# Performance work log

Measured on AMD Instinct MI355X. Metric: run time of the kernel, lower is better.

The kernel has to match this reference:

```python
import jax, jax.numpy as jnp
import numpy as np

K = 4096          # in_features
N = 11008         # out_features
GROUP = 128       # scale group size along K
PACK = 16
BATCH, SEQ = 2, 4096


def setup_inputs() -> dict:
    key = jax.random.key(0)
    k1, k2, k3, k4 = jax.random.split(key, 4)
    x = jax.random.normal(k1, (BATCH, SEQ, K), dtype=jnp.float16)
    # valid ternary codes in {0,1,2} encoding w = code - 1 in {-1,0,+1}
    codes = jax.random.randint(k2, (K, N), 0, 3, dtype=jnp.int32)
    codes = codes.reshape(K // PACK, PACK, N)
    shifts = (2 * jnp.arange(PACK, dtype=jnp.int32))[None, :, None]
    packed_weight = jnp.sum(codes << shifts, axis=1).astype(jnp.int32)  # (K//16, N)
    scales = (jax.random.uniform(k3, (K // GROUP, N), dtype=jnp.float32) * 0.1 + 0.01).astype(jnp.float16)
    bias = (jax.random.normal(k4, (N,), dtype=jnp.float32) * 0.01).astype(jnp.float16)
    return {"x": x, "packed_weight": packed_weight, "scales": scales, "bias": bias}


def _dequant(packed_weight, scales):
    # unpack 16 two-bit codes per int32 along K
    shifts = (2 * jnp.arange(PACK, dtype=jnp.int32))[None, :, None]
    codes = (packed_weight[:, None, :] >> shifts) & 3        # (K//16, 16, N)
    Kp = packed_weight.shape[0] * PACK
    Nn = packed_weight.shape[1]
    w = (codes.astype(jnp.float16) - jnp.float16(1.0)).reshape(Kp, Nn)  # ternary {-1,0,1}
    scale_full = jnp.repeat(scales, GROUP, axis=0)            # (K, N) group-wise gamma
    return w * scale_full


def reference(x, packed_weight, scales, bias):
    Kp = packed_weight.shape[0] * PACK
    Nn = packed_weight.shape[1]
    w = _dequant(packed_weight, scales)                       # (K, N) fp16
    x2 = x.reshape(-1, Kp).astype(jnp.float16)                # (M, K)
    out = jnp.dot(x2, w, preferred_element_type=jnp.float32).astype(jnp.float16)
    out = out + bias
    return out.reshape(*x.shape[:-1], Nn)
```

## Files before the change

### kernel.cpp

```cpp
#include <hip/hip_runtime.h>
#include <stdint.h>

#define K_DIM 4096
#define N_DIM 11008
#define M_DIM 8192
#define BM 256
#define BN 128
#define BK 64
#define NSLAB (K_DIM / BK)
#define BSTRIDE 72

#define FBM 128
#define FBK 32
#define FASTRIDE 32
#define FBSTRIDE 40

typedef _Float16 half8  __attribute__((ext_vector_type(8)));
typedef _Float16 half2v __attribute__((ext_vector_type(2)));
typedef float    floatx4 __attribute__((ext_vector_type(4)));

#define WS_NEEDED ((size_t)M_DIM * K_DIM * 2)

__device__ __forceinline__ void async_lds16(const void* g, void* l) {
    __builtin_amdgcn_global_load_lds(
        (const __attribute__((address_space(1))) uint32_t*)g,
        (__attribute__((address_space(3))) uint32_t*)l, 16, 0, 0);
}

__global__ __launch_bounds__(256) void cvt_a(const float* __restrict__ x,
                                             _Float16* __restrict__ xh) {
    const size_t i = ((size_t)blockIdx.x * 256 + threadIdx.x) * 8;
    const float4 a = *(const float4*)(x + i);
    const float4 b = *(const float4*)(x + i + 4);
    half8 h;
    h[0] = (_Float16)a.x; h[1] = (_Float16)a.y; h[2] = (_Float16)a.z; h[3] = (_Float16)a.w;
    h[4] = (_Float16)b.x; h[5] = (_Float16)b.y; h[6] = (_Float16)b.z; h[7] = (_Float16)b.w;
    *(half8*)(xh + i) = h;
}

__global__ __launch_bounds__(512, 4) void ternary_gemm_hy(
    const _Float16* __restrict__ xh,
    const int*   __restrict__ pw,
    const float* __restrict__ scales,
    const float* __restrict__ bias,
    float*       __restrict__ out)
{
    __shared__ __align__(16) _Float16 lds_a[BM * BK];
    __shared__ __align__(16) _Float16 lds_b[BN * BSTRIDE];

    const int tid  = threadIdx.x;
    const int lane = tid & 63;
    const int wave = tid >> 6;

    const int n0 = blockIdx.x * BN;
    const int m0 = blockIdx.y * BM;
    const int wm = (wave & 3) * 64;
    const int wn = (wave >> 2) * 64;

    const _Float16* ga[4];
    _Float16* la[4];
    #pragma unroll
    for (int i = 0; i < 4; ++i) {
        const int idx = tid + i * 512;
        const int row = idx >> 3;
        const int c   = idx & 7;
        ga[i] = xh + (size_t)(m0 + row) * K_DIM + ((c ^ (row & 7)) * 8);
        la[i] = lds_a + idx * 8;
    }

    const int nb = tid >> 2;
    const int kp = tid & 3;
    const int*   pwp = pw + (size_t)kp * N_DIM + n0 + nb;
    const float* scp = scales + n0 + nb;
    _Float16* bl = lds_b + nb * BSTRIDE + kp * 16;

    floatx4 acc[4][4];
    #pragma unroll
    for (int i = 0; i < 4; ++i)
        #pragma unroll
        for (int j = 0; j < 4; ++j)
            acc[i][j] = floatx4{0.f, 0.f, 0.f, 0.f};

    const int lr = lane & 15;
    const int g  = lane >> 4;
    const int qk = g * 8;
    const int r7 = lr & 7;

    int abase[4], bbase[4];
    #pragma unroll
    for (int t = 0; t < 4; ++t) {
        abase[t] = (wm + t * 16 + lr) * BK;
        bbase[t] = (wn + t * 16 + lr) * BSTRIDE + qk;
    }

    for (int slab = 0; slab < NSLAB; ++slab) {
        const int k0 = slab * BK;

        #pragma unroll
        for (int i = 0; i < 4; ++i)
            async_lds16(ga[i] + k0, la[i]);

        uint32_t v  = (uint32_t)pwp[(size_t)slab * 4 * N_DIM];
        _Float16 sh = (_Float16)scp[(size_t)(slab >> 1) * N_DIM];
        uint32_t sbits = (uint32_t)__builtin_bit_cast(unsigned short, sh);
        uint32_t tmpl = sbits | (((sbits >> 8) ^ 0x80u) << 24);

        uint32_t q[8];
        #pragma unroll
        for (int j = 0; j < 8; ++j) {
            uint32_t t4 = (v >> (4 * j)) & 0xFu;
            uint32_t sp = (t4 | (t4 << 14)) & 0x00030003u;
            uint32_t sel = ((sp & 0x00010001u) << 1) | ((0x00030003u - sp) << 8);
            q[j] = __builtin_amdgcn_perm(tmpl, tmpl, sel);
        }
        *(uint4*)(bl)     = make_uint4(q[0], q[1], q[2], q[3]);
        *(uint4*)(bl + 8) = make_uint4(q[4], q[5], q[6], q[7]);

        __syncthreads();

        #pragma unroll
        for (int h = 0; h < 2; ++h) {
            half8 af[4], bfr[4];
            #pragma unroll
            for (int t = 0; t < 4; ++t) {
                af[t]  = *(const half8*)&lds_a[abase[t] + (((h * 4 + g) ^ r7) * 8)];
                bfr[t] = *(const half8*)&lds_b[bbase[t] + h * 32];
            }
            #pragma unroll
            for (int mt = 0; mt < 4; ++mt)
                #pragma unroll
                for (int nt = 0; nt < 4; ++nt)
                    acc[mt][nt] = __builtin_amdgcn_mfma_f32_16x16x32_f16(
                        af[mt], bfr[nt], acc[mt][nt], 0, 0, 0);
        }

        __syncthreads();
    }

    float bv[4];
    #pragma unroll
    for (int nt = 0; nt < 4; ++nt) bv[nt] = bias[n0 + wn + nt * 16 + lr];

    const int rbase = g * 4;
    #pragma unroll
    for (int mt = 0; mt < 4; ++mt) {
        #pragma unroll
        for (int nt = 0; nt < 4; ++nt) {
            const int col = n0 + wn + nt * 16 + lr;
            float* op = out + (size_t)(m0 + wm + mt * 16 + rbase) * N_DIM + col;
            floatx4 a = acc[mt][nt];
            #pragma unroll
            for (int r = 0; r < 4; ++r)
                op[(size_t)r * N_DIM] = a[r] + bv[nt];
        }
    }
}

__global__ __launch_bounds__(256, 2) void ternary_gemm(
    const float* __restrict__ x,
    const int*   __restrict__ pw,
    const float* __restrict__ scales,
    const float* __restrict__ bias,
    float*       __restrict__ out)
{
    __shared__ __align__(16) _Float16 lds_a[FBM * FASTRIDE];
    __shared__ __align__(16) _Float16 lds_b[FBM * FBSTRIDE];

    const int tid  = threadIdx.x;
    const int lane = tid & 63;
    const int wave = tid >> 6;

    const int n0 = blockIdx.x * FBM;
    const int m0 = blockIdx.y * FBM;

    const int wm = (wave & 1) * 64;
    const int wn = (wave >> 1) * 64;

    const int nb  = tid & 127;
    const int kpi = tid >> 7;
    const int*   pwp = pw + (size_t)kpi * N_DIM + n0 + nb;
    const float* scp = scales + n0 + nb;
    _Float16* bl = lds_b + nb * FBSTRIDE + kpi * 16;

    floatx4 acc[4][4];
    #pragma unroll
    for (int i = 0; i < 4; ++i)
        #pragma unroll
        for (int j = 0; j < 4; ++j)
            acc[i][j] = floatx4{0.f, 0.f, 0.f, 0.f};

    const int lr = lane & 15;
    const int qk = (lane >> 4) * 8;

    for (int slab = 0; slab < K_DIM / FBK; ++slab) {
        const int k0 = slab * FBK;

        #pragma unroll
        for (int i = 0; i < 4; ++i) {
            const int idx = tid + i * 256;
            const int row = idx >> 3;
            const int kq  = (idx & 7) * 4;
            float4 v4 = *(const float4*)(x + (size_t)(m0 + row) * K_DIM + k0 + kq);
            half2v h0; h0[0] = (_Float16)v4.x; h0[1] = (_Float16)v4.y;
            half2v h1; h1[0] = (_Float16)v4.z; h1[1] = (_Float16)v4.w;
            *(uint2*)(lds_a + row * FASTRIDE + kq) =
                make_uint2(__builtin_bit_cast(uint32_t, h0),
                           __builtin_bit_cast(uint32_t, h1));
        }

        uint32_t v  = (uint32_t)pwp[(size_t)slab * 2 * N_DIM];
        _Float16 sh = (_Float16)scp[(size_t)(slab >> 2) * N_DIM];
        uint32_t sbits = (uint32_t)__builtin_bit_cast(unsigned short, sh);
        uint32_t tmpl = sbits | (((sbits >> 8) ^ 0x80u) << 24);

        uint32_t q[8];
        #pragma unroll
        for (int j = 0; j < 8; ++j) {
            uint32_t t4 = (v >> (4 * j)) & 0xFu;
            uint32_t sp = (t4 | (t4 << 14)) & 0x00030003u;
            uint32_t sel = ((sp & 0x00010001u) << 1) | ((0x00030003u - sp) << 8);
            q[j] = __builtin_amdgcn_perm(tmpl, tmpl, sel);
        }
        *(uint4*)(bl)     = make_uint4(q[0], q[1], q[2], q[3]);
        *(uint4*)(bl + 8) = make_uint4(q[4], q[5], q[6], q[7]);

        __syncthreads();

        half8 af[4], bfr[4];
        #pragma unroll
        for (int t = 0; t < 4; ++t) {
            af[t]  = *(const half8*)&lds_a[(wm + t * 16 + lr) * FASTRIDE + qk];
            bfr[t] = *(const half8*)&lds_b[(wn + t * 16 + lr) * FBSTRIDE + qk];
        }
        #pragma unroll
        for (int mt = 0; mt < 4; ++mt)
            #pragma unroll
            for (int nt = 0; nt < 4; ++nt)
                acc[mt][nt] = __builtin_amdgcn_mfma_f32_16x16x32_f16(
                    af[mt], bfr[nt], acc[mt][nt], 0, 0, 0);

        __syncthreads();
    }

    float bv[4];
    #pragma unroll
    for (int nt = 0; nt < 4; ++nt) bv[nt] = bias[n0 + wn + nt * 16 + lr];

    const int rbase = (lane >> 4) * 4;
    #pragma unroll
    for (int mt = 0; mt < 4; ++mt) {
        #pragma unroll
        for (int nt = 0; nt < 4; ++nt) {
            const int col = n0 + wn + nt * 16 + lr;
            float* op = out + (size_t)(m0 + wm + mt * 16 + rbase) * N_DIM + col;
            floatx4 a = acc[mt][nt];
            #pragma unroll
            for (int r = 0; r < 4; ++r)
                op[(size_t)r * N_DIM] = a[r] + bv[nt];
        }
    }
}

extern "C" void kernel_launch(void* const* d_in, const int* in_sizes, int n_in,
                              void* d_out, int out_size, void* d_ws, size_t ws_size,
                              hipStream_t stream) {
    const float* x  = (const float*)d_in[0];
    const int*   pw = (const int*)d_in[1];
    const float* sc = (const float*)d_in[2];
    const float* bs = (const float*)d_in[3];
    float* out = (float*)d_out;

    if (d_ws != nullptr && ws_size >= WS_NEEDED) {
        _Float16* xh = (_Float16*)d_ws;
        cvt_a<<<dim3((unsigned)((size_t)M_DIM * K_DIM / (256 * 8))), 256, 0, stream>>>(x, xh);
        ternary_gemm_hy<<<dim3(N_DIM / BN, M_DIM / BM), 512, 0, stream>>>(xh, pw, sc, bs, out);
    } else {
        ternary_gemm<<<dim3(N_DIM / FBM, M_DIM / FBM), 256, 0, stream>>>(x, pw, sc, bs, out);
    }
}
```

Before: 1.128 ms.

## Double-buffer LDS with 256x256 tiles, weight prefetch and grid swizzle

Replaces the single-buffered 256x128 GEMM with a 256x256-tile kernel. It double-buffers both the A and B LDS tiles and prefetches packed ternary weights and scales two slabs ahead in registers. Each iteration's global-to-LDS loads and weight unpacking now overlap with MFMA work on the other buffer, using fine-grained vmcnt waits instead of two full barriers per slab. It also adds an XOR-swizzled B layout in place of a padded stride, a 1D grid swizzle for L2 locality, and raised MFMA priority. In exchange it uses about 128KB of LDS and more accumulator registers per block, which lowers occupancy to roughly one workgroup per CU.

After: 1.269 ms. +12.5%, slower.

```diff
diff --git a/kernel.cpp b/kernel.cpp
--- a/kernel.cpp
+++ b/kernel.cpp
@@ -5,10 +5,12 @@
 #define N_DIM 11008
 #define M_DIM 8192
 #define BM 256
-#define BN 128
+#define BN 256
 #define BK 64
 #define NSLAB (K_DIM / BK)
-#define BSTRIDE 72
+#define ABUF (BM * BK)
+#define BBUF (BN * BK)
+#define NWG ((N_DIM / BN) * (M_DIM / BM))
 
 #define FBM 128
 #define FBK 32
@@ -38,74 +40,60 @@
     *(half8*)(xh + i) = h;
 }
 
-__global__ __launch_bounds__(512, 4) void ternary_gemm_hy(
+__global__ __launch_bounds__(512, 2) void ternary_gemm_db(
     const _Float16* __restrict__ xh,
     const int*   __restrict__ pw,
     const float* __restrict__ scales,
     const float* __restrict__ bias,
     float*       __restrict__ out)
 {
-    __shared__ __align__(16) _Float16 lds_a[BM * BK];
-    __shared__ __align__(16) _Float16 lds_b[BN * BSTRIDE];
+    __shared__ __align__(16) _Float16 lds_a[2 * ABUF];
+    __shared__ __align__(16) _Float16 lds_b[2 * BBUF];
 
     const int tid  = threadIdx.x;
     const int lane = tid & 63;
-    const int wave = tid >> 6;
-
-    const int n0 = blockIdx.x * BN;
-    const int m0 = blockIdx.y * BM;
-    const int wm = (wave & 3) * 64;
-    const int wn = (wave >> 2) * 64;
-
-    const _Float16* ga[4];
-    _Float16* la[4];
-    #pragma unroll
-    for (int i = 0; i < 4; ++i) {
-        const int idx = tid + i * 512;
-        const int row = idx >> 3;
-        const int c   = idx & 7;
-        ga[i] = xh + (size_t)(m0 + row) * K_DIM + ((c ^ (row & 7)) * 8);
-        la[i] = lds_a + idx * 8;
-    }
-
-    const int nb = tid >> 2;
-    const int kp = tid & 3;
-    const int*   pwp = pw + (size_t)kp * N_DIM + n0 + nb;
+    const int w    = tid >> 6;
+
+    const int bid = blockIdx.x;
+    const int swz = (bid & 7) * (NWG / 8) + (bid >> 3);
+    const int n0 = (swz % (N_DIM / BN)) * BN;
+    const int m0 = (swz / (N_DIM / BN)) * BM;
+
+    const int band = (w & 3) * 64;
+    const int wn   = (w >> 2) * 128;
+
+    const int arow = lane >> 3;
+    const int achk = (lane & 7) ^ arow;
+    const _Float16* gaBase = xh + (size_t)(m0 + band + arow) * K_DIM + achk * 8;
+
+    const int nb = tid >> 1;
+    const int kp = tid & 1;
+    const int* pwp = pw + (size_t)(kp * 2) * N_DIM + n0 + nb;
     const float* scp = scales + n0 + nb;
-    _Float16* bl = lds_b + nb * BSTRIDE + kp * 16;
-
-    floatx4 acc[4][4];
+    const int s7  = nb & 7;
+    const int c0a = ((kp * 2 + 0) * 2 + 0) ^ s7;
+    const int c0b = ((kp * 2 + 0) * 2 + 1) ^ s7;
+    const int c1a = ((kp * 2 + 1) * 2 + 0) ^ s7;
+    const int c1b = ((kp * 2 + 1) * 2 + 1) ^ s7;
+
+    floatx4 acc[4][8];
     #pragma unroll
     for (int i = 0; i < 4; ++i)
         #pragma unroll
-        for (int j = 0; j < 4; ++j)
+        for (int j = 0; j < 8; ++j)
             acc[i][j] = floatx4{0.f, 0.f, 0.f, 0.f};
 
     const int lr = lane & 15;
     const int g  = lane >> 4;
-    const int qk = g * 8;
-    const int r7 = lr & 7;
-
-    int abase[4], bbase[4];
-    #pragma unroll
-    for (int t = 0; t < 4; ++t) {
-        abase[t] = (wm + t * 16 + lr) * BK;
-        bbase[t] = (wn + t * 16 + lr) * BSTRIDE + qk;
-    }
-
-    for (int slab = 0; slab < NSLAB; ++slab) {
-        const int k0 = slab * BK;
-
-        #pragma unroll
-        for (int i = 0; i < 4; ++i)
-            async_lds16(ga[i] + k0, la[i]);
-
-        uint32_t v  = (uint32_t)pwp[(size_t)slab * 4 * N_DIM];
-        _Float16 sh = (_Float16)scp[(size_t)(slab >> 1) * N_DIM];
-        uint32_t sbits = (uint32_t)__builtin_bit_cast(unsigned short, sh);
-        uint32_t tmpl = sbits | (((sbits >> 8) ^ 0x80u) << 24);
-
-        uint32_t q[8];
+    const int x7 = lr & 7;
+
+    int aoff[4], boff[8];
+    #pragma unroll
+    for (int mt = 0; mt < 4; ++mt) aoff[mt] = (band + mt * 16 + lr) * BK;
+    #pragma unroll
+    for (int nt = 0; nt < 8; ++nt) boff[nt] = (wn + nt * 16 + lr) * BK;
+
+    auto permq = [](uint32_t v, uint32_t tmpl, uint32_t* q) {
         #pragma unroll
         for (int j = 0; j < 8; ++j) {
             uint32_t t4 = (v >> (4 * j)) & 0xFu;
@@ -113,41 +101,95 @@
             uint32_t sel = ((sp & 0x00010001u) << 1) | ((0x00030003u - sp) << 8);
             q[j] = __builtin_amdgcn_perm(tmpl, tmpl, sel);
         }
-        *(uint4*)(bl)     = make_uint4(q[0], q[1], q[2], q[3]);
-        *(uint4*)(bl + 8) = make_uint4(q[4], q[5], q[6], q[7]);
-
-        __syncthreads();
-
+    };
+    auto stage_b = [&](uint32_t v0, uint32_t v1, float scf, _Float16* rowb) {
+        _Float16 sh = (_Float16)scf;
+        uint32_t sbits = (uint32_t)__builtin_bit_cast(unsigned short, sh);
+        uint32_t tmpl = sbits | (((sbits >> 8) ^ 0x80u) << 24);
+        uint32_t q[8];
+        permq(v0, tmpl, q);
+        *(uint4*)(rowb + c0a * 8) = make_uint4(q[0], q[1], q[2], q[3]);
+        *(uint4*)(rowb + c0b * 8) = make_uint4(q[4], q[5], q[6], q[7]);
+        permq(v1, tmpl, q);
+        *(uint4*)(rowb + c1a * 8) = make_uint4(q[0], q[1], q[2], q[3]);
+        *(uint4*)(rowb + c1b * 8) = make_uint4(q[4], q[5], q[6], q[7]);
+    };
+    auto stage_a = [&](int slab, int buf) {
+        const _Float16* gk = gaBase + slab * BK;
+        _Float16* dst = lds_a + buf * ABUF + band * BK;
+        #pragma unroll
+        for (int i = 0; i < 8; ++i)
+            async_lds16(gk + (size_t)i * 8 * K_DIM, dst + i * 8 * BK);
+    };
+
+    uint32_t pv00 = (uint32_t)pwp[0];
+    uint32_t pv01 = (uint32_t)pwp[(size_t)1 * N_DIM];
+    float    sc0  = scp[0];
+    uint32_t pvA0 = (uint32_t)pwp[(size_t)4 * N_DIM];
+    uint32_t pvA1 = (uint32_t)pwp[(size_t)5 * N_DIM];
+    float    scA  = scp[0];
+    stage_a(0, 0);
+    stage_b(pv00, pv01, sc0, lds_b + nb * BK);
+    asm volatile("s_waitcnt lgkmcnt(0)" ::: "memory");
+    __builtin_amdgcn_s_barrier();
+
+    uint32_t pvB0 = 0, pvB1 = 0; float scB = 0.f;
+
+    for (int t = 0; t < NSLAB; ++t) {
+        const int cur = t & 1;
+
+        if (t + 2 < NSLAB) {
+            pvB0 = (uint32_t)pwp[(size_t)((t + 2) * 4 + 0) * N_DIM];
+            pvB1 = (uint32_t)pwp[(size_t)((t + 2) * 4 + 1) * N_DIM];
+            scB  = scp[(size_t)((t + 2) >> 1) * N_DIM];
+        }
+        if (t + 1 < NSLAB) {
+            stage_a(t + 1, cur ^ 1);
+            stage_b(pvA0, pvA1, scA, lds_b + (cur ^ 1) * BBUF + nb * BK);
+        }
+
+        if (t + 2 < NSLAB)      asm volatile("s_waitcnt vmcnt(11)" ::: "memory");
+        else if (t + 1 < NSLAB) asm volatile("s_waitcnt vmcnt(8)"  ::: "memory");
+        else                    asm volatile("s_waitcnt vmcnt(0)"  ::: "memory");
+
+        const _Float16* Ab = lds_a + cur * ABUF;
+        const _Float16* Bb = lds_b + cur * BBUF;
+        __builtin_amdgcn_s_setprio(1);
         #pragma unroll
         for (int h = 0; h < 2; ++h) {
-            half8 af[4], bfr[4];
-            #pragma unroll
-            for (int t = 0; t < 4; ++t) {
-                af[t]  = *(const half8*)&lds_a[abase[t] + (((h * 4 + g) ^ r7) * 8)];
-                bfr[t] = *(const half8*)&lds_b[bbase[t] + h * 32];
-            }
+            const int co = ((h * 4 + g) ^ x7) * 8;
+            half8 af[4], bf[8];
+            #pragma unroll
+            for (int mt = 0; mt < 4; ++mt) af[mt] = *(const half8*)&Ab[aoff[mt] + co];
+            #pragma unroll
+            for (int nt = 0; nt < 8; ++nt) bf[nt] = *(const half8*)&Bb[boff[nt] + co];
             #pragma unroll
             for (int mt = 0; mt < 4; ++mt)
                 #pragma unroll
-                for (int nt = 0; nt < 4; ++nt)
+                for (int nt = 0; nt < 8; ++nt)
                     acc[mt][nt] = __builtin_amdgcn_mfma_f32_16x16x32_f16(
-                        af[mt], bfr[nt], acc[mt][nt], 0, 0, 0);
-        }
-
-        __syncthreads();
-    }
-
-    float bv[4];
-    #pragma unroll
-    for (int nt = 0; nt < 4; ++nt) bv[nt] = bias[n0 + wn + nt * 16 + lr];
+                        af[mt], bf[nt], acc[mt][nt], 0, 0, 0);
+        }
+        __builtin_amdgcn_s_setprio(0);
+
+        if (t + 1 < NSLAB) {
+            asm volatile("s_waitcnt lgkmcnt(0)" ::: "memory");
+            __builtin_amdgcn_s_barrier();
+        }
+        pvA0 = pvB0; pvA1 = pvB1; scA = scB;
+    }
+
+    float bv[8];
+    #pragma unroll
+    for (int nt = 0; nt < 8; ++nt) bv[nt] = bias[n0 + wn + nt * 16 + lr];
 
     const int rbase = g * 4;
     #pragma unroll
     for (int mt = 0; mt < 4; ++mt) {
         #pragma unroll
-        for (int nt = 0; nt < 4; ++nt) {
+        for (int nt = 0; nt < 8; ++nt) {
             const int col = n0 + wn + nt * 16 + lr;
-            float* op = out + (size_t)(m0 + wm + mt * 16 + rbase) * N_DIM + col;
+            float* op = out + (size_t)(m0 + band + mt * 16 + rbase) * N_DIM + col;
             floatx4 a = acc[mt][nt];
             #pragma unroll
             for (int r = 0; r < 4; ++r)
@@ -273,7 +315,7 @@
     if (d_ws != nullptr && ws_size >= WS_NEEDED) {
         _Float16* xh = (_Float16*)d_ws;
         cvt_a<<<dim3((unsigned)((size_t)M_DIM * K_DIM / (256 * 8))), 256, 0, stream>>>(x, xh);
-        ternary_gemm_hy<<<dim3(N_DIM / BN, M_DIM / BM), 512, 0, stream>>>(xh, pw, sc, bs, out);
+        ternary_gemm_db<<<dim3(NWG), 512, 0, stream>>>(xh, pw, sc, bs, out);
     } else {
         ternary_gemm<<<dim3(N_DIM / FBM, M_DIM / FBM), 256, 0, stream>>>(x, pw, sc, bs, out);
     }
```

## Switch to 32x32x16 MFMA, XOR-swizzled B tile, block-id remap, prefetch weights

Applied to the files above, without the earlier changes.

Replaces the 4x4 grid of 16x16x32 MFMAs per wave with a 2x2 grid of 32x32x16 MFMAs. This reduces LDS fragment loads per MFMA and the instruction count. The padded B tile in LDS becomes an XOR-swizzled layout that matches the A swizzle, which avoids bank conflicts without padding. The grid becomes 1D with a block-id remap that groups blocks for L2 reuse. The packed weight and scale for the next slab are now loaded one iteration ahead to hide global latency. The epilogue is rewritten for the 32x32 accumulator layout, which changes the output store pattern.

Result: slower. 1.183 ms (+4.8%).

```diff
diff --git a/kernel.cpp b/kernel.cpp
--- a/kernel.cpp
+++ b/kernel.cpp
@@ -8,16 +8,19 @@
 #define BN 128
 #define BK 64
 #define NSLAB (K_DIM / BK)
-#define BSTRIDE 72
+#define NBN (N_DIM / BN)
+#define NBM (M_DIM / BM)
+#define NWG (NBN * NBM)
 
 #define FBM 128
 #define FBK 32
 #define FASTRIDE 32
 #define FBSTRIDE 40
 
-typedef _Float16 half8  __attribute__((ext_vector_type(8)));
-typedef _Float16 half2v __attribute__((ext_vector_type(2)));
+typedef _Float16 half8   __attribute__((ext_vector_type(8)));
+typedef _Float16 half2v  __attribute__((ext_vector_type(2)));
 typedef float    floatx4 __attribute__((ext_vector_type(4)));
+typedef float    floatx16 __attribute__((ext_vector_type(16)));
 
 #define WS_NEEDED ((size_t)M_DIM * K_DIM * 2)
 
@@ -38,7 +41,7 @@
     *(half8*)(xh + i) = h;
 }
 
-__global__ __launch_bounds__(512, 4) void ternary_gemm_hy(
+__global__ __launch_bounds__(512, 4) void ternary_gemm_w3(
     const _Float16* __restrict__ xh,
     const int*   __restrict__ pw,
     const float* __restrict__ scales,
@@ -46,16 +49,19 @@
     float*       __restrict__ out)
 {
     __shared__ __align__(16) _Float16 lds_a[BM * BK];
-    __shared__ __align__(16) _Float16 lds_b[BN * BSTRIDE];
+    __shared__ __align__(16) _Float16 lds_b[BN * BK];
 
     const int tid  = threadIdx.x;
     const int lane = tid & 63;
-    const int wave = tid >> 6;
-
-    const int n0 = blockIdx.x * BN;
-    const int m0 = blockIdx.y * BM;
-    const int wm = (wave & 3) * 64;
-    const int wn = (wave >> 2) * 64;
+    const int w    = tid >> 6;
+
+    const int bid = blockIdx.x;
+    const int swz = (bid & 7) * (NWG / 8) + (bid >> 3);
+    const int m0 = (swz / NBN) * BM;
+    const int n0 = (swz % NBN) * BN;
+
+    const int wm = (w & 3) * 64;
+    const int wn = (w >> 2) * 64;
 
     const _Float16* ga[4];
     _Float16* la[4];
@@ -70,88 +76,93 @@
 
     const int nb = tid >> 2;
     const int kp = tid & 3;
-    const int*   pwp = pw + (size_t)kp * N_DIM + n0 + nb;
+    const int* pwp = pw + (size_t)kp * N_DIM + n0 + nb;
     const float* scp = scales + n0 + nb;
-    _Float16* bl = lds_b + nb * BSTRIDE + kp * 16;
-
-    floatx4 acc[4][4];
-    #pragma unroll
-    for (int i = 0; i < 4; ++i)
-        #pragma unroll
-        for (int j = 0; j < 4; ++j)
-            acc[i][j] = floatx4{0.f, 0.f, 0.f, 0.f};
-
-    const int lr = lane & 15;
-    const int g  = lane >> 4;
-    const int qk = g * 8;
-    const int r7 = lr & 7;
-
-    int abase[4], bbase[4];
-    #pragma unroll
-    for (int t = 0; t < 4; ++t) {
-        abase[t] = (wm + t * 16 + lr) * BK;
-        bbase[t] = (wn + t * 16 + lr) * BSTRIDE + qk;
-    }
-
-    for (int slab = 0; slab < NSLAB; ++slab) {
-        const int k0 = slab * BK;
-
+    const int s7 = nb & 7;
+    const int cA = (kp * 2 + 0) ^ s7;
+    const int cB = (kp * 2 + 1) ^ s7;
+    _Float16* bl = lds_b + nb * BK;
+
+    floatx16 acc[2][2];
+    #pragma unroll
+    for (int i = 0; i < 2; ++i)
+        #pragma unroll
+        for (int j = 0; j < 2; ++j)
+            acc[i][j] = (floatx16)(0.f);
+
+    const int l31 = lane & 31;
+    const int h5  = lane >> 5;
+    const int r7  = l31 & 7;
+
+    const int aoff0 = (wm +  0 + l31) * BK;
+    const int aoff1 = (wm + 32 + l31) * BK;
+    const int boff0 = (wn +  0 + l31) * BK;
+    const int boff1 = (wn + 32 + l31) * BK;
+
+    uint32_t pv = (uint32_t)pwp[0];
+    float    sv = scp[0];
+
+    for (int t = 0; t < NSLAB; ++t) {
         #pragma unroll
         for (int i = 0; i < 4; ++i)
-            async_lds16(ga[i] + k0, la[i]);
-
-        uint32_t v  = (uint32_t)pwp[(size_t)slab * 4 * N_DIM];
-        _Float16 sh = (_Float16)scp[(size_t)(slab >> 1) * N_DIM];
-        uint32_t sbits = (uint32_t)__builtin_bit_cast(unsigned short, sh);
-        uint32_t tmpl = sbits | (((sbits >> 8) ^ 0x80u) << 24);
-
-        uint32_t q[8];
-        #pragma unroll
-        for (int j = 0; j < 8; ++j) {
-            uint32_t t4 = (v >> (4 * j)) & 0xFu;
-            uint32_t sp = (t4 | (t4 << 14)) & 0x00030003u;
-            uint32_t sel = ((sp & 0x00010001u) << 1) | ((0x00030003u - sp) << 8);
-            q[j] = __builtin_amdgcn_perm(tmpl, tmpl, sel);
-        }
-        *(uint4*)(bl)     = make_uint4(q[0], q[1], q[2], q[3]);
-        *(uint4*)(bl + 8) = make_uint4(q[4], q[5], q[6], q[7]);
-
-        __syncthreads();
-
-        #pragma unroll
-        for (int h = 0; h < 2; ++h) {
-            half8 af[4], bfr[4];
-            #pragma unroll
-            for (int t = 0; t < 4; ++t) {
-                af[t]  = *(const half8*)&lds_a[abase[t] + (((h * 4 + g) ^ r7) * 8)];
-                bfr[t] = *(const half8*)&lds_b[bbase[t] + h * 32];
+            async_lds16(ga[i] + t * BK, la[i]);
+
+        uint32_t pvN = pv; float svN = sv;
+        if (t + 1 < NSLAB) {
+            pvN = (uint32_t)pwp[(size_t)(t + 1) * 4 * N_DIM];
+            svN = scp[(size_t)((t + 1) >> 1) * N_DIM];
+        }
+
+        {
+            _Float16 sh = (_Float16)sv;
+            uint32_t sbits = (uint32_t)__builtin_bit_cast(unsigned short, sh);
+            uint32_t tmpl = sbits | (((sbits >> 8) ^ 0x80u) << 24);
+            uint32_t q[8];
+            #pragma unroll
+            for (int j = 0; j < 8; ++j) {
+                uint32_t t4 = (pv >> (4 * j)) & 0xFu;
+                uint32_t sp = (t4 | (t4 << 14)) & 0x00030003u;
+                uint32_t sel = ((sp & 0x00010001u) << 1) | ((0x00030003u - sp) << 8);
+                q[j] = __builtin_amdgcn_perm(tmpl, tmpl, sel);
             }
-            #pragma unroll
-            for (int mt = 0; mt < 4; ++mt)
-                #pragma unroll
-                for (int nt = 0; nt < 4; ++nt)
-                    acc[mt][nt] = __builtin_amdgcn_mfma_f32_16x16x32_f16(
-                        af[mt], bfr[nt], acc[mt][nt], 0, 0, 0);
-        }
-
-        __syncthreads();
-    }
-
-    float bv[4];
-    #pragma unroll
-    for (int nt = 0; nt < 4; ++nt) bv[nt] = bias[n0 + wn + nt * 16 + lr];
-
-    const int rbase = g * 4;
-    #pragma unroll
-    for (int mt = 0; mt < 4; ++mt) {
-        #pragma unroll
-        for (int nt = 0; nt < 4; ++nt) {
-            const int col = n0 + wn + nt * 16 + lr;
-            float* op = out + (size_t)(m0 + wm + mt * 16 + rbase) * N_DIM + col;
-            floatx4 a = acc[mt][nt];
-            #pragma unroll
-            for (int r = 0; r < 4; ++r)
-                op[(size_t)r * N_DIM] = a[r] + bv[nt];
+            *(uint4*)(bl + cA * 8) = make_uint4(q[0], q[1], q[2], q[3]);
+            *(uint4*)(bl + cB * 8) = make_uint4(q[4], q[5], q[6], q[7]);
+        }
+
+        __syncthreads();
+
+        #pragma unroll
+        for (int ks = 0; ks < 4; ++ks) {
+            const int ck = ((ks * 2 + h5) ^ r7) * 8;
+            half8 af0 = *(const half8*)&lds_a[aoff0 + ck];
+            half8 af1 = *(const half8*)&lds_a[aoff1 + ck];
+            half8 bf0 = *(const half8*)&lds_b[boff0 + ck];
+            half8 bf1 = *(const half8*)&lds_b[boff1 + ck];
+            acc[0][0] = __builtin_amdgcn_mfma_f32_32x32x16_f16(af0, bf0, acc[0][0], 0, 0, 0);
+            acc[0][1] = __builtin_amdgcn_mfma_f32_32x32x16_f16(af0, bf1, acc[0][1], 0, 0, 0);
+            acc[1][0] = __builtin_amdgcn_mfma_f32_32x32x16_f16(af1, bf0, acc[1][0], 0, 0, 0);
+            acc[1][1] = __builtin_amdgcn_mfma_f32_32x32x16_f16(af1, bf1, acc[1][1], 0, 0, 0);
+        }
+
+        __syncthreads();
+        pv = pvN; sv = svN;
+    }
+
+    float bvE[2];
+    #pragma unroll
+    for (int nt = 0; nt < 2; ++nt) bvE[nt] = bias[n0 + wn + nt * 32 + l31];
+
+    #pragma unroll
+    for (int mt = 0; mt < 2; ++mt) {
+        #pragma unroll
+        for (int nt = 0; nt < 2; ++nt) {
+            const int col = n0 + wn + nt * 32 + l31;
+            const floatx16 a = acc[mt][nt];
+            #pragma unroll
+            for (int reg = 0; reg < 16; ++reg) {
+                const int row = m0 + wm + mt * 32 + (reg & 3) + 8 * (reg >> 2) + 4 * h5;
+                out[(size_t)row * N_DIM + col] = a[reg] + bvE[nt];
+            }
         }
     }
 }
@@ -273,7 +284,7 @@
     if (d_ws != nullptr && ws_size >= WS_NEEDED) {
         _Float16* xh = (_Float16*)d_ws;
         cvt_a<<<dim3((unsigned)((size_t)M_DIM * K_DIM / (256 * 8))), 256, 0, stream>>>(x, xh);
-        ternary_gemm_hy<<<dim3(N_DIM / BN, M_DIM / BM), 512, 0, stream>>>(xh, pw, sc, bs, out);
+        ternary_gemm_w3<<<dim3(NWG), 512, 0, stream>>>(xh, pw, sc, bs, out);
     } else {
         ternary_gemm<<<dim3(N_DIM / FBM, M_DIM / FBM), 256, 0, stream>>>(x, pw, sc, bs, out);
     }
```

## Double-buffer A tile in LDS, prefetch packed weights, and swizzle workgroup order

Applied to the files above, without the earlier changes.

The main GEMM now double-buffers the activation tile in LDS, issuing the async global-to-LDS loads for the next K slab before computing the current one. It also prefetches the packed weights and scales two slabs ahead in registers. The loop uses explicit vmcnt/lgkmcnt waits and raw s_barrier in place of __syncthreads. The B tile drops its padded stride for an XOR-swizzled layout, the launch becomes a 1D grid remapped for L2 locality, and s_setprio raises priority during the MFMA section. The costs are extra LDS for the second A buffer and hand-tuned wait counts that must match the number of outstanding loads exactly.

Measured after the change: 1.070 ms, median of 2. -5.2%, faster.

```diff
diff --git a/kernel.cpp b/kernel.cpp
--- a/kernel.cpp
+++ b/kernel.cpp
@@ -8,15 +8,18 @@
 #define BN 128
 #define BK 64
 #define NSLAB (K_DIM / BK)
-#define BSTRIDE 72
+#define NBN (N_DIM / BN)
+#define NBM (M_DIM / BM)
+#define NWG (NBN * NBM)
+#define ABUF (BM * BK)
 
 #define FBM 128
 #define FBK 32
 #define FASTRIDE 32
 #define FBSTRIDE 40
 
-typedef _Float16 half8  __attribute__((ext_vector_type(8)));
-typedef _Float16 half2v __attribute__((ext_vector_type(2)));
+typedef _Float16 half8   __attribute__((ext_vector_type(8)));
+typedef _Float16 half2v  __attribute__((ext_vector_type(2)));
 typedef float    floatx4 __attribute__((ext_vector_type(4)));
 
 #define WS_NEEDED ((size_t)M_DIM * K_DIM * 2)
@@ -38,41 +41,47 @@
     *(half8*)(xh + i) = h;
 }
 
-__global__ __launch_bounds__(512, 4) void ternary_gemm_hy(
+__global__ __launch_bounds__(512, 4) void ternary_gemm_p2(
     const _Float16* __restrict__ xh,
     const int*   __restrict__ pw,
     const float* __restrict__ scales,
     const float* __restrict__ bias,
     float*       __restrict__ out)
 {
-    __shared__ __align__(16) _Float16 lds_a[BM * BK];
-    __shared__ __align__(16) _Float16 lds_b[BN * BSTRIDE];
+    __shared__ __align__(16) _Float16 lds_a[2 * ABUF];
+    __shared__ __align__(16) _Float16 lds_b[BN * BK];
 
     const int tid  = threadIdx.x;
     const int lane = tid & 63;
-    const int wave = tid >> 6;
-
-    const int n0 = blockIdx.x * BN;
-    const int m0 = blockIdx.y * BM;
-    const int wm = (wave & 3) * 64;
-    const int wn = (wave >> 2) * 64;
+    const int w    = tid >> 6;
+
+    const int bid = blockIdx.x;
+    const int swz = (bid & 7) * (NWG / 8) + (bid >> 3);
+    const int m0 = (swz / NBN) * BM;
+    const int n0 = (swz % NBN) * BN;
+
+    const int band = (w & 3) * 64;
+    const int wn   = (w >> 2) * 64;
 
     const _Float16* ga[4];
-    _Float16* la[4];
+    int laOff[4];
     #pragma unroll
     for (int i = 0; i < 4; ++i) {
         const int idx = tid + i * 512;
         const int row = idx >> 3;
         const int c   = idx & 7;
-        ga[i] = xh + (size_t)(m0 + row) * K_DIM + ((c ^ (row & 7)) * 8);
-        la[i] = lds_a + idx * 8;
+        ga[i]    = xh + (size_t)(m0 + row) * K_DIM + ((c ^ (row & 7)) * 8);
+        laOff[i] = idx * 8;
     }
 
     const int nb = tid >> 2;
     const int kp = tid & 3;
-    const int*   pwp = pw + (size_t)kp * N_DIM + n0 + nb;
+    const int* pwp = pw + (size_t)kp * N_DIM + n0 + nb;
     const float* scp = scales + n0 + nb;
-    _Float16* bl = lds_b + nb * BSTRIDE + kp * 16;
+    const int s7 = nb & 7;
+    const int cA = (kp * 2 + 0) ^ s7;
+    const int cB = (kp * 2 + 1) ^ s7;
+    _Float16* bl = lds_b + nb * BK;
 
     floatx4 acc[4][4];
     #pragma unroll
@@ -83,28 +92,24 @@
 
     const int lr = lane & 15;
     const int g  = lane >> 4;
-    const int qk = g * 8;
-    const int r7 = lr & 7;
-
-    int abase[4], bbase[4];
+    const int x7 = lr & 7;
+
+    int aoff[4], boff[4];
     #pragma unroll
     for (int t = 0; t < 4; ++t) {
-        abase[t] = (wm + t * 16 + lr) * BK;
-        bbase[t] = (wn + t * 16 + lr) * BSTRIDE + qk;
-    }
-
-    for (int slab = 0; slab < NSLAB; ++slab) {
-        const int k0 = slab * BK;
-
+        aoff[t] = (band + t * 16 + lr) * BK;
+        boff[t] = (wn   + t * 16 + lr) * BK;
+    }
+
+    auto stage_a = [&](int t, int buf) {
         #pragma unroll
         for (int i = 0; i < 4; ++i)
-            async_lds16(ga[i] + k0, la[i]);
-
-        uint32_t v  = (uint32_t)pwp[(size_t)slab * 4 * N_DIM];
-        _Float16 sh = (_Float16)scp[(size_t)(slab >> 1) * N_DIM];
+            async_lds16(ga[i] + t * BK, lds_a + buf * ABUF + laOff[i]);
+    };
+    auto stage_b = [&](uint32_t v, float scf) {
+        _Float16 sh = (_Float16)scf;
         uint32_t sbits = (uint32_t)__builtin_bit_cast(unsigned short, sh);
         uint32_t tmpl = sbits | (((sbits >> 8) ^ 0x80u) << 24);
-
         uint32_t q[8];
         #pragma unroll
         for (int j = 0; j < 8; ++j) {
@@ -113,18 +118,44 @@
             uint32_t sel = ((sp & 0x00010001u) << 1) | ((0x00030003u - sp) << 8);
             q[j] = __builtin_amdgcn_perm(tmpl, tmpl, sel);
         }
-        *(uint4*)(bl)     = make_uint4(q[0], q[1], q[2], q[3]);
-        *(uint4*)(bl + 8) = make_uint4(q[4], q[5], q[6], q[7]);
-
-        __syncthreads();
-
+        *(uint4*)(bl + cA * 8) = make_uint4(q[0], q[1], q[2], q[3]);
+        *(uint4*)(bl + cB * 8) = make_uint4(q[4], q[5], q[6], q[7]);
+    };
+
+    stage_a(0, 0);
+    uint32_t pv0 = (uint32_t)pwp[0];
+    float    sv0 = scp[0];
+    uint32_t pv1 = (uint32_t)pwp[(size_t)4 * N_DIM];
+    float    sv1 = scp[0];
+
+    for (int t = 0; t < NSLAB; ++t) {
+        const int cur = t & 1;
+
+        if (t + 1 < NSLAB) stage_a(t + 1, cur ^ 1);
+        uint32_t pv2 = 0; float sv2 = 0.f;
+        if (t + 2 < NSLAB) {
+            pv2 = (uint32_t)pwp[(size_t)(t + 2) * 4 * N_DIM];
+            sv2 = scp[(size_t)((t + 2) >> 1) * N_DIM];
+        }
+        stage_b(pv0, sv0);
+
+        if (t + 2 < NSLAB)      asm volatile("s_waitcnt vmcnt(6)" ::: "memory");
+        else if (t + 1 < NSLAB) asm volatile("s_waitcnt vmcnt(4)" ::: "memory");
+        else                    asm volatile("s_waitcnt vmcnt(0)" ::: "memory");
+        asm volatile("s_waitcnt lgkmcnt(0)" ::: "memory");
+        __builtin_amdgcn_sched_barrier(0);
+        __builtin_amdgcn_s_barrier();
+
+        const _Float16* Ab = lds_a + cur * ABUF;
+        __builtin_amdgcn_s_setprio(1);
         #pragma unroll
         for (int h = 0; h < 2; ++h) {
+            const int co = ((h * 4 + g) ^ x7) * 8;
             half8 af[4], bfr[4];
             #pragma unroll
-            for (int t = 0; t < 4; ++t) {
-                af[t]  = *(const half8*)&lds_a[abase[t] + (((h * 4 + g) ^ r7) * 8)];
-                bfr[t] = *(const half8*)&lds_b[bbase[t] + h * 32];
+            for (int tt = 0; tt < 4; ++tt) {
+                af[tt]  = *(const half8*)&Ab[aoff[tt] + co];
+                bfr[tt] = *(const half8*)&lds_b[boff[tt] + co];
             }
             #pragma unroll
             for (int mt = 0; mt < 4; ++mt)
@@ -133,8 +164,13 @@
                     acc[mt][nt] = __builtin_amdgcn_mfma_f32_16x16x32_f16(
                         af[mt], bfr[nt], acc[mt][nt], 0, 0, 0);
         }
-
-        __syncthreads();
+        __builtin_amdgcn_s_setprio(0);
+
+        asm volatile("s_waitcnt lgkmcnt(0)" ::: "memory");
+        __builtin_amdgcn_sched_barrier(0);
+        __builtin_amdgcn_s_barrier();
+
+        pv0 = pv1; sv0 = sv1; pv1 = pv2; sv1 = sv2;
     }
 
     float bv[4];
@@ -147,7 +183,7 @@
         #pragma unroll
         for (int nt = 0; nt < 4; ++nt) {
             const int col = n0 + wn + nt * 16 + lr;
-            float* op = out + (size_t)(m0 + wm + mt * 16 + rbase) * N_DIM + col;
+            float* op = out + (size_t)(m0 + band + mt * 16 + rbase) * N_DIM + col;
             floatx4 a = acc[mt][nt];
             #pragma unroll
             for (int r = 0; r < 4; ++r)
@@ -273,7 +309,7 @@
     if (d_ws != nullptr && ws_size >= WS_NEEDED) {
         _Float16* xh = (_Float16*)d_ws;
         cvt_a<<<dim3((unsigned)((size_t)M_DIM * K_DIM / (256 * 8))), 256, 0, stream>>>(x, xh);
-        ternary_gemm_hy<<<dim3(N_DIM / BN, M_DIM / BM), 512, 0, stream>>>(xh, pw, sc, bs, out);
+        ternary_gemm_p2<<<dim3(NWG), 512, 0, stream>>>(xh, pw, sc, bs, out);
     } else {
         ternary_gemm<<<dim3(N_DIM / FBM, M_DIM / FBM), 256, 0, stream>>>(x, pw, sc, bs, out);
     }
```
